# Optimization experiments

Measured on AMD Instinct MI355X. Metric: run time of the kernel, lower is better.

## Reference

```python
import jax, jax.numpy as jnp
import numpy as np
from jax import lax

W_SCALE = 0.1   # brevitas SignedBinaryWeightPerTensorConst default scaling_init
A_SCALE = 1.0   # SignedBinaryActPerTensorConst: min/max = -1/1 -> scale 1
BN_EPS = 1e-5


def _bin_w(w):
    # sign(w) * const scale, straight-through estimator (identity STE as in brevitas binary_sign_ste)
    q = jnp.where(w >= 0, W_SCALE, -W_SCALE).astype(w.dtype)
    return w + lax.stop_gradient(q - w)


def _bin_act(x):
    # QuantHardTanh with binary act quant: output is sign(x)*1, STE passes grad inside [-1,1]
    c = jnp.clip(x, -A_SCALE, A_SCALE)
    q = jnp.where(x >= 0, A_SCALE, -A_SCALE).astype(x.dtype)
    return c + lax.stop_gradient(q - c)


def _conv(x, w, b, stride=(1, 1), pad=((0, 0), (0, 0))):
    y = lax.conv_general_dilated(x, _bin_w(w), window_strides=stride, padding=pad,
                                 dimension_numbers=('NCHW', 'OIHW', 'NCHW'))
    return y + b[None, :, None, None]


def _bn(x, gamma, beta):
    # training-mode BatchNorm2d: batch statistics over (N, H, W)
    mu = jnp.mean(x, axis=(0, 2, 3), keepdims=True)
    var = jnp.var(x, axis=(0, 2, 3), keepdims=True)
    inv = lax.rsqrt(var + BN_EPS)
    return (x - mu) * inv * gamma[None, :, None, None] + beta[None, :, None, None]


def _pool2x1(x):
    # MaxPool2d((2,1)) with floor: drop trailing odd row
    N, C, H, W = x.shape
    h2 = H // 2
    return x[:, :, : 2 * h2].reshape(N, C, h2, 2, W).max(axis=3)


def setup_inputs() -> dict:
    key = jax.random.key(0)
    ks = jax.random.split(key, 10)
    nC = 128
    d = {
        'x':  jax.random.normal(ks[0], (64, 1, 16000, 1), jnp.float32),
        'w1': jax.random.normal(ks[1], (nC, 1, 84, 1), jnp.float32) * 0.05,
        'b1': jnp.zeros((nC,), jnp.float32),
        'g1': jnp.ones((nC,), jnp.float32), 'be1': jnp.zeros((nC,), jnp.float32),
        'w2': jax.random.normal(ks[2], (nC, nC, 4, 1), jnp.float32) * 0.05,
        'b2': jnp.zeros((nC,), jnp.float32),
        'g2': jnp.ones((nC,), jnp.float32), 'be2': jnp.zeros((nC,), jnp.float32),
        'w3': jax.random.normal(ks[3], (2 * nC, nC, 4, 1), jnp.float32) * 0.05,
        'b3': jnp.zeros((2 * nC,), jnp.float32),
        'g3': jnp.ones((2 * nC,), jnp.float32), 'be3': jnp.zeros((2 * nC,), jnp.float32),
        'w5': jax.random.normal(ks[4], (4 * nC, 2 * nC, 3, 1), jnp.float32) * 0.05,
        'b5': jnp.zeros((4 * nC,), jnp.float32),
        'g5': jnp.ones((4 * nC,), jnp.float32), 'be5': jnp.zeros((4 * nC,), jnp.float32),
        'wfc': jax.random.normal(ks[5], (35, 4 * nC * 249), jnp.float32) * 0.01,
    }
    return d


def reference(x, w1, b1, g1, be1, w2, b2, g2, be2, w3, b3, g3, be3,
              w5, b5, g5, be5, wfc):
    h = _conv(x, w1, b1, stride=(4, 1))                     # [B,128,3980,1]
    h = _pool2x1(_bin_act(_bn(h, g1, be1)))                 # [B,128,1990,1]
    h = _conv(h, w2, b2, pad=((2, 2), (0, 0)))              # [B,128,1991,1]
    h = _pool2x1(_bin_act(_bn(h, g2, be2)))                 # [B,128,995,1]
    h = _conv(h, w3, b3, pad=((1, 1), (0, 0)))              # [B,256,994,1]
    h = _pool2x1(_bin_act(_bn(h, g3, be3)))                 # [B,256,497,1]
    h = _conv(h, w5, b5, pad=((2, 2), (0, 0)))              # [B,512,499,1]
    h = _pool2x1(_bin_act(_bn(h, g5, be5)))                 # [B,512,249,1]
    h = h.reshape(h.shape[0], -1)                           # [B, 512*249]
    return h @ _bin_w(wfc).T                                # [B, 35]
```

## Files before the change

kernel.cpp:

```cpp
#include <hip/hip_runtime.h>
#include <stdint.h>


constexpr int Bn  = 64;
constexpr int H1  = 3980;
constexpr int J1  = 1990;
constexpr int H2o = 1991, J2 = 995;
constexpr int H3o = 994,  J3 = 497;
constexpr int H5o = 499,  J5 = 249;
constexpr int FCW = 249 * 8;

__global__ void binarize_all(const float* __restrict__ w2, const float* __restrict__ w3,
                             const float* __restrict__ w5, const float* __restrict__ w1,
                             uint64_t* __restrict__ wb2, uint64_t* __restrict__ wb3,
                             uint64_t* __restrict__ wb5, float* __restrict__ w1pk)
{
    int idx = blockIdx.x * 256 + threadIdx.x;
    if (idx < 1024) {
        int wdx = idx & 1, k = (idx >> 1) & 3, c = idx >> 3;
        uint64_t v = 0;
        for (int ci = 0; ci < 64; ++ci)
            if (w2[((size_t)c * 128 + (wdx * 64 + ci)) * 4 + k] >= 0.f) v |= 1ull << ci;
        wb2[idx] = v;
    } else if (idx < 3072) {
        int t = idx - 1024;
        int wdx = t & 1, k = (t >> 1) & 3, c = t >> 3;
        uint64_t v = 0;
        for (int ci = 0; ci < 64; ++ci)
            if (w3[((size_t)c * 128 + (wdx * 64 + ci)) * 4 + k] >= 0.f) v |= 1ull << ci;
        wb3[t] = v;
    } else if (idx < 9216) {
        int t = idx - 3072;
        int wdx = t & 3, k = (t >> 2) % 3, c = t / 12;
        uint64_t v = 0;
        for (int ci = 0; ci < 64; ++ci)
            if (w5[((size_t)c * 256 + (wdx * 64 + ci)) * 3 + k] >= 0.f) v |= 1ull << ci;
        wb5[t] = v;
    } else if (idx < 9216 + 10752) {
        int t  = idx - 9216;
        int G  = t / 672, r = t % 672;
        int kg = r >> 5;
        int e  = r & 31;
        int u  = e >> 2, jj = e & 3;
        w1pk[t] = (w1[(size_t)(G * 8 + u) * 84 + kg * 4 + jj] >= 0.f) ? 0.1f : -0.1f;
    }
}

__global__ __launch_bounds__(256) void binarize_fc(const float* __restrict__ wfc,
                                                   uint64_t* __restrict__ wbf)
{
    const int oc = blockIdx.x, wdx = blockIdx.y;
    const int wave = threadIdx.x >> 6, lane = threadIdx.x & 63;
    const int hh = wave * 64 + lane;
    const bool ok = hh < 249;
    const float* src = wfc + (size_t)oc * 127488 + (size_t)wdx * 64 * 249 + hh;
    uint64_t word = 0;
    #pragma unroll 8
    for (int c = 0; c < 64; ++c) {
        const float v = ok ? src[(size_t)c * 249] : -1.f;
        if (v >= 0.f) word |= 1ull << c;
    }
    if (ok) wbf[(size_t)oc * FCW + (size_t)hh * 8 + wdx] = word;
}

#define ROW_FMA(A, XV) \
    A[u] = fmaf(wv.x, XV.x, A[u]); A[u] = fmaf(wv.y, XV.y, A[u]); \
    A[u] = fmaf(wv.z, XV.z, A[u]); A[u] = fmaf(wv.w, XV.w, A[u]);
#define ROW_STAT(A, HOFF) { \
    const int h = h0 + (HOFF) + tid; \
    if (h < H1) { const float v = A[u] + bv; base[h] = v; \
                  s += (double)v; q += (double)v * v; } }

__global__ __launch_bounds__(256) void conv1_y1(
    const float* __restrict__ x, const float4* __restrict__ w1pk,
    const float* __restrict__ b1, float* __restrict__ y1,
    double2* __restrict__ part)
{
    __shared__ float4 xs4[2068];
    __shared__ float4 wl[336];
    __shared__ double2 statw[4][16];
    const int n   = blockIdx.y;
    const int bh  = blockIdx.x;
    const int h0  = bh << 11;
    const int z   = blockIdx.z;
    const int tid = threadIdx.x;
    const int wave = tid >> 6, lane = tid & 63;

    const float4* x4 = (const float4*)x + (size_t)n * 4000;
    for (int i = tid; i < 2068; i += 256) {
        const int gi = h0 + i;
        xs4[i] = (gi < 4000) ? x4[gi] : make_float4(0.f, 0.f, 0.f, 0.f);
    }
    const float4* wsrc = w1pk + (size_t)z * 336;
    for (int i = tid; i < 336; i += 256) wl[i] = wsrc[i];
    __syncthreads();

    for (int g = 0; g < 2; ++g) {
        float a0[8] = {0,0,0,0,0,0,0,0};
        float a1r[8] = {0,0,0,0,0,0,0,0};
        float a2[8] = {0,0,0,0,0,0,0,0};
        float a3[8] = {0,0,0,0,0,0,0,0};
        float a4[8] = {0,0,0,0,0,0,0,0};
        float a5[8] = {0,0,0,0,0,0,0,0};
        float a6[8] = {0,0,0,0,0,0,0,0};
        float a7[8] = {0,0,0,0,0,0,0,0};
        #pragma unroll 3
        for (int kg = 0; kg < 21; ++kg) {
            const float4 xv0 = xs4[tid + kg];
            const float4 xv1 = xs4[tid + 256 + kg];
            const float4 xv2 = xs4[tid + 512 + kg];
            const float4 xv3 = xs4[tid + 768 + kg];
            const float4 xv4 = xs4[tid + 1024 + kg];
            const float4 xv5 = xs4[tid + 1280 + kg];
            const float4 xv6 = xs4[tid + 1536 + kg];
            const float4 xv7 = xs4[tid + 1792 + kg];
            const float4* wk = &wl[(g * 21 + kg) * 8];
            #pragma unroll
            for (int u = 0; u < 8; ++u) {
                const float4 wv = wk[u];
                ROW_FMA(a0, xv0)
                ROW_FMA(a1r, xv1)
                ROW_FMA(a2, xv2)
                ROW_FMA(a3, xv3)
                ROW_FMA(a4, xv4)
                ROW_FMA(a5, xv5)
                ROW_FMA(a6, xv6)
                ROW_FMA(a7, xv7)
            }
        }
        #pragma unroll
        for (int u = 0; u < 8; ++u) {
            const int c = z * 16 + g * 8 + u;
            const float bv = b1[c];
            float* base = y1 + ((size_t)n * 128 + c) * H1;
            double s = 0.0, q = 0.0;
            ROW_STAT(a0, 0)
            ROW_STAT(a1r, 256)
            ROW_STAT(a2, 512)
            ROW_STAT(a3, 768)
            ROW_STAT(a4, 1024)
            ROW_STAT(a5, 1280)
            ROW_STAT(a6, 1536)
            ROW_STAT(a7, 1792)
            #pragma unroll
            for (int o = 32; o > 0; o >>= 1) {
                s += __shfl_xor(s, o, 64);
                q += __shfl_xor(q, o, 64);
            }
            if (lane == 0) statw[wave][g * 8 + u] = make_double2(s, q);
        }
    }
    __syncthreads();
    if (tid < 16) {
        const double2 p0 = statw[0][tid], p1v = statw[1][tid];
        const double2 p2 = statw[2][tid], p3  = statw[3][tid];
        part[((size_t)((n * 2 + bh) * 8 + z)) * 16 + tid] =
            make_double2(((p0.x + p1v.x) + p2.x) + p3.x,
                         ((p0.y + p1v.y) + p2.y) + p3.y);
    }
}

__global__ __launch_bounds__(128) void bn_reduce1(const double2* __restrict__ part,
                                                  float2* __restrict__ bnp)
{
    __shared__ double sS[128], sQ[128];
    const int c = blockIdx.x, t = threadIdx.x;
    const int z = c >> 4, cl = c & 15;
    const double2 p = part[((size_t)(t * 8 + z)) * 16 + cl];
    sS[t] = p.x; sQ[t] = p.y;
    __syncthreads();
    for (int o = 64; o > 0; o >>= 1) {
        if (t < o) { sS[t] += sS[t + o]; sQ[t] += sQ[t + o]; }
        __syncthreads();
    }
    if (t == 0) {
        const double N = (double)Bn * H1;
        const double mu  = sS[0] / N;
        const double var = sQ[0] / N - mu * mu;
        bnp[c] = make_float2((float)mu, (float)(1.0 / sqrt(var + 1e-5)));
    }
}

__global__ __launch_bounds__(256) void signpool1_y(
    const float* __restrict__ y1, const float2* __restrict__ bnp,
    const float* __restrict__ g1, const float* __restrict__ be1,
    uint64_t* __restrict__ a1)
{
    __shared__ float2 smi[128];
    __shared__ float  sg[128], sbe[128];
    const int n   = blockIdx.y;
    const int tid = threadIdx.x;
    if (tid < 128) { smi[tid] = bnp[tid]; sg[tid] = g1[tid]; sbe[tid] = be1[tid]; }
    __syncthreads();
    const int j2   = blockIdx.x * 128 + (tid & 127);
    const int half = tid >> 7;
    if (j2 >= 995) return;
    uint64_t wa = 0, wb = 0;
    for (int i = 0; i < 64; ++i) {
        const int c = half * 64 + i;
        const float4 v = *(const float4*)(y1 + ((size_t)n * 128 + c) * H1 + 4 * j2);
        const float2 mi = smi[c];
        const float gg = sg[c], bb = sbe[c];
        const float t0 = __fadd_rn(__fmul_rn(__fmul_rn(__fsub_rn(v.x, mi.x), mi.y), gg), bb);
        const float t1 = __fadd_rn(__fmul_rn(__fmul_rn(__fsub_rn(v.y, mi.x), mi.y), gg), bb);
        const float t2 = __fadd_rn(__fmul_rn(__fmul_rn(__fsub_rn(v.z, mi.x), mi.y), gg), bb);
        const float t3 = __fadd_rn(__fmul_rn(__fmul_rn(__fsub_rn(v.w, mi.x), mi.y), gg), bb);
        if ((t0 >= 0.f) || (t1 >= 0.f)) wa |= 1ull << i;
        if ((t2 >= 0.f) || (t3 >= 0.f)) wb |= 1ull << i;
    }
    uint64_t* dst = a1 + ((size_t)n * J1 + 2 * j2) * 2 + half;
    dst[0] = wa;
    dst[2] = wb;
}

template<int CINW, int KK, int PAD, int COUT>
__global__ __launch_bounds__(COUT) void bconv_stats(
    const uint64_t* __restrict__ ain, const uint64_t* __restrict__ wb,
    const int HIN, const int HOUT, int* __restrict__ part)
{
    __shared__ uint64_t rows[(64 + KK - 1) * CINW];
    const int n  = blockIdx.y;
    const int h0 = blockIdx.x << 6;
    const int c  = threadIdx.x;
    for (int i = c; i < (64 + KK - 1) * CINW; i += COUT) {
        int r = h0 - PAD + i / CINW;
        rows[i] = (r >= 0 && r < HIN) ? ain[((size_t)n * HIN + r) * CINW + (i % CINW)] : 0ull;
    }
    __syncthreads();
    uint64_t wreg[KK * CINW];
    #pragma unroll
    for (int i = 0; i < KK * CINW; ++i) wreg[i] = wb[(size_t)c * KK * CINW + i];
    int pcw[KK];
    #pragma unroll
    for (int k = 0; k < KK; ++k) {
        int pc = 0;
        #pragma unroll
        for (int wd = 0; wd < CINW; ++wd) pc += __popcll(wreg[k * CINW + wd]);
        pcw[k] = pc;
    }
    int sq = 0, sq2 = 0;
    const int hmax = min(64, HOUT - h0);
    for (int i = 0; i < hmax; ++i) {
        const int h = h0 + i;
        int X = 0;
        #pragma unroll
        for (int k = 0; k < KK; ++k)
            #pragma unroll
            for (int wd = 0; wd < CINW; ++wd)
                X += __popcll(rows[(i + k) * CINW + wd] ^ wreg[k * CINW + wd]);
        int q = 64 * CINW * KK - 2 * X;
        if (h < PAD || h > HIN + PAD - KK) {
            #pragma unroll
            for (int k = 0; k < KK; ++k)
                if (k < PAD - h || k >= HIN + PAD - h)
                    q -= 64 * CINW - 2 * pcw[k];
        }
        sq += q; sq2 += q * q;
    }
    const size_t blk = (size_t)n * gridDim.x + blockIdx.x;
    part[(blk * COUT + c) * 2 + 0] = sq;
    part[(blk * COUT + c) * 2 + 1] = sq2;
}

template<int CINW, int KK, int PAD, int COUT>
__global__ __launch_bounds__(COUT) void bconv_sign(
    const uint64_t* __restrict__ ain, const uint64_t* __restrict__ wb,
    const int HIN, const int HOUT, const int J,
    const float* __restrict__ bias, const float2* __restrict__ bnp,
    const float* __restrict__ g, const float* __restrict__ be,
    uint64_t* __restrict__ aout)
{
    constexpr int W = COUT / 64;
    __shared__ uint64_t rows[(64 + KK - 1) * CINW];
    const int n  = blockIdx.y;
    const int h0 = blockIdx.x << 6;
    const int c  = threadIdx.x;
    for (int i = c; i < (64 + KK - 1) * CINW; i += COUT) {
        int r = h0 - PAD + i / CINW;
        rows[i] = (r >= 0 && r < HIN) ? ain[((size_t)n * HIN + r) * CINW + (i % CINW)] : 0ull;
    }
    __syncthreads();
    uint64_t wreg[KK * CINW];
    #pragma unroll
    for (int i = 0; i < KK * CINW; ++i) wreg[i] = wb[(size_t)c * KK * CINW + i];
    int pcw[KK];
    #pragma unroll
    for (int k = 0; k < KK; ++k) {
        int pc = 0;
        #pragma unroll
        for (int wd = 0; wd < CINW; ++wd) pc += __popcll(wreg[k * CINW + wd]);
        pcw[k] = pc;
    }
    const float bb = bias[c], gg = g[c], bbe = be[c];
    const float2 mi = bnp[c];
    const int wv = c >> 6, lane = c & 63;
    uint64_t prev = 0;
    const int hmax = min(64, HOUT - h0);
    for (int i = 0; i < hmax; ++i) {
        const int h = h0 + i;
        int X = 0;
        #pragma unroll
        for (int k = 0; k < KK; ++k)
            #pragma unroll
            for (int wd = 0; wd < CINW; ++wd)
                X += __popcll(rows[(i + k) * CINW + wd] ^ wreg[k * CINW + wd]);
        int q = 64 * CINW * KK - 2 * X;
        if (h < PAD || h > HIN + PAD - KK) {
            #pragma unroll
            for (int k = 0; k < KK; ++k)
                if (k < PAD - h || k >= HIN + PAD - h)
                    q -= 64 * CINW - 2 * pcw[k];
        }
        const float y = __fadd_rn(__fmul_rn(0.1f, (float)q), bb);
        const float t = __fadd_rn(__fmul_rn(__fmul_rn(__fsub_rn(y, mi.x), mi.y), gg), bbe);
        const uint64_t word = __ballot(t >= 0.f);
        if (i & 1) {
            const int j = h >> 1;
            if (lane == 0 && j < J)
                aout[((size_t)n * J + j) * W + wv] = prev | word;
        } else {
            prev = word;
        }
    }
}

__global__ __launch_bounds__(256) void bn_reduce_q(
    const int* __restrict__ part, const int nblk, const int C,
    const double N, const float* __restrict__ bias, float2* __restrict__ bnp)
{
    __shared__ long long sS[256], sQ[256];
    const int c = blockIdx.x, t = threadIdx.x;
    long long Sq = 0, Sq2 = 0;
    for (int b = t; b < nblk; b += 256) {
        const int2 p = *(const int2*)(part + ((size_t)b * C + c) * 2);
        Sq += p.x; Sq2 += p.y;
    }
    sS[t] = Sq; sQ[t] = Sq2;
    __syncthreads();
    for (int o = 128; o > 0; o >>= 1) {
        if (t < o) { sS[t] += sS[t + o]; sQ[t] += sQ[t + o]; }
        __syncthreads();
    }
    if (t == 0) {
        const double bb = (double)bias[c];
        const double S  = 0.1 * (double)sS[0] + N * bb;
        const double SS = 0.01 * (double)sQ[0] + 0.2 * bb * (double)sS[0] + N * bb * bb;
        const double mu = S / N;
        const double var = SS / N - mu * mu;
        bnp[c] = make_float2((float)mu, (float)(1.0 / sqrt(var + 1e-5)));
    }
}

__global__ void fc_kernel(const uint64_t* __restrict__ a5, const uint64_t* __restrict__ wfcb,
                          float* __restrict__ out)
{
    const int n    = blockIdx.y;
    const int oc   = blockIdx.x * 4 + (threadIdx.x >> 6);
    const int lane = threadIdx.x & 63;
    if (oc >= 35) return;
    const uint64_t* arow = a5   + (size_t)n  * FCW;
    const uint64_t* wrow = wfcb + (size_t)oc * FCW;
    int X = 0;
    for (int i = lane; i < FCW; i += 64)
        X += __popcll(arow[i] ^ wrow[i]);
    for (int o = 32; o > 0; o >>= 1) X += __shfl_xor(X, o, 64);
    if (lane == 0) out[(size_t)n * 35 + oc] = 0.1f * (float)(127488 - 2 * X);
}

extern "C" void kernel_launch(void* const* d_in, const int* in_sizes, int n_in,
                              void* d_out, int out_size, void* d_ws, size_t ws_size,
                              hipStream_t stream)
{
    (void)in_sizes; (void)n_in; (void)out_size;
    const float* x   = (const float*)d_in[0];
    const float* w1  = (const float*)d_in[1];
    const float* b1  = (const float*)d_in[2];
    const float* g1  = (const float*)d_in[3];
    const float* be1 = (const float*)d_in[4];
    const float* w2  = (const float*)d_in[5];
    const float* b2  = (const float*)d_in[6];
    const float* g2  = (const float*)d_in[7];
    const float* be2 = (const float*)d_in[8];
    const float* w3  = (const float*)d_in[9];
    const float* b3  = (const float*)d_in[10];
    const float* g3  = (const float*)d_in[11];
    const float* be3 = (const float*)d_in[12];
    const float* w5  = (const float*)d_in[13];
    const float* b5  = (const float*)d_in[14];
    const float* g5  = (const float*)d_in[15];
    const float* be5 = (const float*)d_in[16];
    const float* wfc = (const float*)d_in[17];
    char* ws = (char*)d_ws;

    size_t cur = 0;
    auto take = [&](size_t bytes) {
        size_t r = cur;
        cur = (cur + bytes + 255) & ~(size_t)255;
        return r;
    };
    const size_t off_y1 = take(130416640);
    float*    y1  = (float*)(ws + off_y1);
    int*      pq  = (int*)(ws + off_y1 + 35651584);
    uint64_t* a1  = (uint64_t*)(ws + take(2037760));
    uint64_t* a2  = (uint64_t*)(ws + take(1018880));
    uint64_t* a3  = (uint64_t*)(ws + take(1017856));
    uint64_t* a5  = (uint64_t*)(ws + take(1019904));
    uint64_t* wb2 = (uint64_t*)(ws + take(8192));
    uint64_t* wb3 = (uint64_t*)(ws + take(16384));
    uint64_t* wb5 = (uint64_t*)(ws + take(49152));
    uint64_t* wbf = (uint64_t*)(ws + take(557760));
    float*    w1pk = (float*)(ws + take(43008));
    double2*  p1  = (double2*)(ws + take(262144));
    float2*   bnp1 = (float2*)(ws + take(1024));
    float2*   bnp2 = (float2*)(ws + take(1024));
    float2*   bnp3 = (float2*)(ws + take(2048));
    float2*   bnp5 = (float2*)(ws + take(4096));
    if (cur > ws_size) return;

    hipLaunchKernelGGL(binarize_all, dim3(78), dim3(256), 0, stream,
                       w2, w3, w5, w1, wb2, wb3, wb5, w1pk);
    hipLaunchKernelGGL(binarize_fc, dim3(35, 8), dim3(256), 0, stream, wfc, wbf);
    hipLaunchKernelGGL(conv1_y1, dim3(2, 64, 8), dim3(256), 0, stream,
                       x, (const float4*)w1pk, b1, y1, p1);
    hipLaunchKernelGGL(bn_reduce1, dim3(128), dim3(128), 0, stream, p1, bnp1);
    hipLaunchKernelGGL(signpool1_y, dim3(8, 64), dim3(256), 0, stream,
                       y1, bnp1, g1, be1, a1);
    hipLaunchKernelGGL((bconv_stats<2, 4, 2, 128>), dim3(32, 64), dim3(128), 0, stream,
                       a1, wb2, J1, H2o, pq);
    hipLaunchKernelGGL(bn_reduce_q, dim3(128), dim3(256), 0, stream,
                       pq, 2048, 128, (double)Bn * H2o, b2, bnp2);
    hipLaunchKernelGGL((bconv_sign<2, 4, 2, 128>), dim3(32, 64), dim3(128), 0, stream,
                       a1, wb2, J1, H2o, J2, b2, bnp2, g2, be2, a2);
    hipLaunchKernelGGL((bconv_stats<2, 4, 1, 256>), dim3(16, 64), dim3(256), 0, stream,
                       a2, wb3, J2, H3o, pq);
    hipLaunchKernelGGL(bn_reduce_q, dim3(256), dim3(256), 0, stream,
                       pq, 1024, 256, (double)Bn * H3o, b3, bnp3);
    hipLaunchKernelGGL((bconv_sign<2, 4, 1, 256>), dim3(16, 64), dim3(256), 0, stream,
                       a2, wb3, J2, H3o, J3, b3, bnp3, g3, be3, a3);
    hipLaunchKernelGGL((bconv_stats<4, 3, 2, 512>), dim3(8, 64), dim3(512), 0, stream,
                       a3, wb5, J3, H5o, pq);
    hipLaunchKernelGGL(bn_reduce_q, dim3(512), dim3(256), 0, stream,
                       pq, 512, 512, (double)Bn * H5o, b5, bnp5);
    hipLaunchKernelGGL((bconv_sign<4, 3, 2, 512>), dim3(8, 64), dim3(512), 0, stream,
                       a3, wb5, J3, H5o, J5, b5, bnp5, g5, be5, a5);
    hipLaunchKernelGGL(fc_kernel, dim3(9, 64), dim3(256), 0, stream,
                       a5, wbf, (float*)d_out);
}
```

Measured before the change: 327.9 us.

## Replace BN reduce kernels with sharded atomics and merge weight prep kernels

The stats kernels now atomically accumulate integer sum and sum-of-squares into 16 sharded 64-bit counters, replacing per-block partial writes. The sign kernels read the shards directly and compute mean and inverse std inline, so the three separate bn_reduce_q launches are removed. The two weight binarization kernels are merged into one prep kernel that also zeroes the accumulators. This cuts four kernel launches and a partial-sum round trip, at the cost of atomic contention and redundant per-block stat recomputation.

```diff
diff --git a/kernel.cpp b/kernel.cpp
--- a/kernel.cpp
+++ b/kernel.cpp
@@ -9,58 +9,68 @@
 constexpr int H3o = 994,  J3 = 497;
 constexpr int H5o = 499,  J5 = 249;
 constexpr int FCW = 249 * 8;
-
-__global__ void binarize_all(const float* __restrict__ w2, const float* __restrict__ w3,
-                             const float* __restrict__ w5, const float* __restrict__ w1,
-                             uint64_t* __restrict__ wb2, uint64_t* __restrict__ wb3,
-                             uint64_t* __restrict__ wb5, float* __restrict__ w1pk)
-{
-    int idx = blockIdx.x * 256 + threadIdx.x;
-    if (idx < 1024) {
-        int wdx = idx & 1, k = (idx >> 1) & 3, c = idx >> 3;
-        uint64_t v = 0;
-        for (int ci = 0; ci < 64; ++ci)
-            if (w2[((size_t)c * 128 + (wdx * 64 + ci)) * 4 + k] >= 0.f) v |= 1ull << ci;
-        wb2[idx] = v;
-    } else if (idx < 3072) {
-        int t = idx - 1024;
-        int wdx = t & 1, k = (t >> 1) & 3, c = t >> 3;
-        uint64_t v = 0;
-        for (int ci = 0; ci < 64; ++ci)
-            if (w3[((size_t)c * 128 + (wdx * 64 + ci)) * 4 + k] >= 0.f) v |= 1ull << ci;
-        wb3[t] = v;
-    } else if (idx < 9216) {
-        int t = idx - 3072;
-        int wdx = t & 3, k = (t >> 2) % 3, c = t / 12;
-        uint64_t v = 0;
-        for (int ci = 0; ci < 64; ++ci)
-            if (w5[((size_t)c * 256 + (wdx * 64 + ci)) * 3 + k] >= 0.f) v |= 1ull << ci;
-        wb5[t] = v;
-    } else if (idx < 9216 + 10752) {
-        int t  = idx - 9216;
-        int G  = t / 672, r = t % 672;
-        int kg = r >> 5;
-        int e  = r & 31;
-        int u  = e >> 2, jj = e & 3;
-        w1pk[t] = (w1[(size_t)(G * 8 + u) * 84 + kg * 4 + jj] >= 0.f) ? 0.1f : -0.1f;
-    }
-}
-
-__global__ __launch_bounds__(256) void binarize_fc(const float* __restrict__ wfc,
-                                                   uint64_t* __restrict__ wbf)
-{
-    const int oc = blockIdx.x, wdx = blockIdx.y;
-    const int wave = threadIdx.x >> 6, lane = threadIdx.x & 63;
-    const int hh = wave * 64 + lane;
-    const bool ok = hh < 249;
-    const float* src = wfc + (size_t)oc * 127488 + (size_t)wdx * 64 * 249 + hh;
-    uint64_t word = 0;
-    #pragma unroll 8
-    for (int c = 0; c < 64; ++c) {
-        const float v = ok ? src[(size_t)c * 249] : -1.f;
-        if (v >= 0.f) word |= 1ull << c;
-    }
-    if (ok) wbf[(size_t)oc * FCW + (size_t)hh * 8 + wdx] = word;
+constexpr int NSH = 16;
+constexpr int QS2 = 0;
+constexpr int QS3 = 4096;
+constexpr int QS5 = 12288;
+constexpr int QS_TOTAL = 28672;
+
+__global__ __launch_bounds__(256) void prep_all(
+    const float* __restrict__ w2, const float* __restrict__ w3,
+    const float* __restrict__ w5, const float* __restrict__ wfc,
+    const float* __restrict__ w1,
+    uint64_t* __restrict__ wb2, uint64_t* __restrict__ wb3,
+    uint64_t* __restrict__ wb5, uint64_t* __restrict__ wbf,
+    float* __restrict__ w1pk, unsigned long long* __restrict__ qs)
+{
+    const int bx  = blockIdx.x;
+    const int idx = bx * 256 + threadIdx.x;
+    if (idx < QS_TOTAL) qs[idx] = 0ull;
+
+    if (bx < 78) {
+        if (idx < 1024) {
+            int wdx = idx & 1, k = (idx >> 1) & 3, c = idx >> 3;
+            uint64_t v = 0;
+            for (int ci = 0; ci < 64; ++ci)
+                if (w2[((size_t)c * 128 + (wdx * 64 + ci)) * 4 + k] >= 0.f) v |= 1ull << ci;
+            wb2[idx] = v;
+        } else if (idx < 3072) {
+            int t = idx - 1024;
+            int wdx = t & 1, k = (t >> 1) & 3, c = t >> 3;
+            uint64_t v = 0;
+            for (int ci = 0; ci < 64; ++ci)
+                if (w3[((size_t)c * 128 + (wdx * 64 + ci)) * 4 + k] >= 0.f) v |= 1ull << ci;
+            wb3[t] = v;
+        } else if (idx < 9216) {
+            int t = idx - 3072;
+            int wdx = t & 3, k = (t >> 2) % 3, c = t / 12;
+            uint64_t v = 0;
+            for (int ci = 0; ci < 64; ++ci)
+                if (w5[((size_t)c * 256 + (wdx * 64 + ci)) * 3 + k] >= 0.f) v |= 1ull << ci;
+            wb5[t] = v;
+        } else if (idx < 9216 + 10752) {
+            int t  = idx - 9216;
+            int G  = t / 672, r = t % 672;
+            int kg = r >> 5;
+            int e  = r & 31;
+            int u  = e >> 2, jj = e & 3;
+            w1pk[t] = (w1[(size_t)(G * 8 + u) * 84 + kg * 4 + jj] >= 0.f) ? 0.1f : -0.1f;
+        }
+    } else {
+        const int t = bx - 78;
+        const int oc = t >> 3, wdx = t & 7;
+        const int wave = threadIdx.x >> 6, lane = threadIdx.x & 63;
+        const int hh = wave * 64 + lane;
+        const bool ok = hh < 249;
+        const float* src = wfc + (size_t)oc * 127488 + (size_t)wdx * 64 * 249 + hh;
+        uint64_t word = 0;
+        #pragma unroll 8
+        for (int c = 0; c < 64; ++c) {
+            const float v = ok ? src[(size_t)c * 249] : -1.f;
+            if (v >= 0.f) word |= 1ull << c;
+        }
+        if (ok) wbf[(size_t)oc * FCW + (size_t)hh * 8 + wdx] = word;
+    }
 }
 
 #define ROW_FMA(A, XV) \
@@ -216,7 +226,7 @@
 template<int CINW, int KK, int PAD, int COUT>
 __global__ __launch_bounds__(COUT) void bconv_stats(
     const uint64_t* __restrict__ ain, const uint64_t* __restrict__ wb,
-    const int HIN, const int HOUT, int* __restrict__ part)
+    const int HIN, const int HOUT, unsigned long long* __restrict__ qs)
 {
     __shared__ uint64_t rows[(64 + KK - 1) * CINW];
     const int n  = blockIdx.y;
@@ -257,16 +267,16 @@
         }
         sq += q; sq2 += q * q;
     }
-    const size_t blk = (size_t)n * gridDim.x + blockIdx.x;
-    part[(blk * COUT + c) * 2 + 0] = sq;
-    part[(blk * COUT + c) * 2 + 1] = sq2;
+    const int sh = (blockIdx.x + blockIdx.y) & (NSH - 1);
+    atomicAdd(&qs[((size_t)sh * COUT + c) * 2 + 0], (unsigned long long)(long long)sq);
+    atomicAdd(&qs[((size_t)sh * COUT + c) * 2 + 1], (unsigned long long)(long long)sq2);
 }
 
 template<int CINW, int KK, int PAD, int COUT>
 __global__ __launch_bounds__(COUT) void bconv_sign(
     const uint64_t* __restrict__ ain, const uint64_t* __restrict__ wb,
-    const int HIN, const int HOUT, const int J,
-    const float* __restrict__ bias, const float2* __restrict__ bnp,
+    const int HIN, const int HOUT, const int J, const double N,
+    const float* __restrict__ bias, const unsigned long long* __restrict__ qs,
     const float* __restrict__ g, const float* __restrict__ be,
     uint64_t* __restrict__ aout)
 {
@@ -279,6 +289,18 @@
         int r = h0 - PAD + i / CINW;
         rows[i] = (r >= 0 && r < HIN) ? ain[((size_t)n * HIN + r) * CINW + (i % CINW)] : 0ull;
     }
+    long long Sq = 0, Sq2 = 0;
+    #pragma unroll
+    for (int s = 0; s < NSH; ++s) {
+        Sq  += (long long)qs[((size_t)s * COUT + c) * 2 + 0];
+        Sq2 += (long long)qs[((size_t)s * COUT + c) * 2 + 1];
+    }
+    const double bb_d = (double)bias[c];
+    const double S  = 0.1 * (double)Sq + N * bb_d;
+    const double SS = 0.01 * (double)Sq2 + 0.2 * bb_d * (double)Sq + N * bb_d * bb_d;
+    const double mu = S / N;
+    const double var = SS / N - mu * mu;
+    const float2 mi = make_float2((float)mu, (float)(1.0 / sqrt(var + 1e-5)));
     __syncthreads();
     uint64_t wreg[KK * CINW];
     #pragma unroll
@@ -292,7 +314,6 @@
         pcw[k] = pc;
     }
     const float bb = bias[c], gg = g[c], bbe = be[c];
-    const float2 mi = bnp[c];
     const int wv = c >> 6, lane = c & 63;
     uint64_t prev = 0;
     const int hmax = min(64, HOUT - h0);
@@ -321,33 +342,6 @@
         } else {
             prev = word;
         }
-    }
-}
-
-__global__ __launch_bounds__(256) void bn_reduce_q(
-    const int* __restrict__ part, const int nblk, const int C,
-    const double N, const float* __restrict__ bias, float2* __restrict__ bnp)
-{
-    __shared__ long long sS[256], sQ[256];
-    const int c = blockIdx.x, t = threadIdx.x;
-    long long Sq = 0, Sq2 = 0;
-    for (int b = t; b < nblk; b += 256) {
-        const int2 p = *(const int2*)(part + ((size_t)b * C + c) * 2);
-        Sq += p.x; Sq2 += p.y;
-    }
-    sS[t] = Sq; sQ[t] = Sq2;
-    __syncthreads();
-    for (int o = 128; o > 0; o >>= 1) {
-        if (t < o) { sS[t] += sS[t + o]; sQ[t] += sQ[t + o]; }
-        __syncthreads();
-    }
-    if (t == 0) {
-        const double bb = (double)bias[c];
-        const double S  = 0.1 * (double)sS[0] + N * bb;
-        const double SS = 0.01 * (double)sQ[0] + 0.2 * bb * (double)sS[0] + N * bb * bb;
-        const double mu = S / N;
-        const double var = SS / N - mu * mu;
-        bnp[c] = make_float2((float)mu, (float)(1.0 / sqrt(var + 1e-5)));
     }
 }
 
@@ -400,7 +394,6 @@
     };
     const size_t off_y1 = take(130416640);
     float*    y1  = (float*)(ws + off_y1);
-    int*      pq  = (int*)(ws + off_y1 + 35651584);
     uint64_t* a1  = (uint64_t*)(ws + take(2037760));
     uint64_t* a2  = (uint64_t*)(ws + take(1018880));
     uint64_t* a3  = (uint64_t*)(ws + take(1017856));
@@ -411,38 +404,29 @@
     uint64_t* wbf = (uint64_t*)(ws + take(557760));
     float*    w1pk = (float*)(ws + take(43008));
     double2*  p1  = (double2*)(ws + take(262144));
+    unsigned long long* qs = (unsigned long long*)(ws + take(QS_TOTAL * 8));
     float2*   bnp1 = (float2*)(ws + take(1024));
-    float2*   bnp2 = (float2*)(ws + take(1024));
-    float2*   bnp3 = (float2*)(ws + take(2048));
-    float2*   bnp5 = (float2*)(ws + take(4096));
     if (cur > ws_size) return;
 
-    hipLaunchKernelGGL(binarize_all, dim3(78), dim3(256), 0, stream,
-                       w2, w3, w5, w1, wb2, wb3, wb5, w1pk);
-    hipLaunchKernelGGL(binarize_fc, dim3(35, 8), dim3(256), 0, stream, wfc, wbf);
+    hipLaunchKernelGGL(prep_all, dim3(358), dim3(256), 0, stream,
+                       w2, w3, w5, wfc, w1, wb2, wb3, wb5, wbf, w1pk, qs);
     hipLaunchKernelGGL(conv1_y1, dim3(2, 64, 8), dim3(256), 0, stream,
                        x, (const float4*)w1pk, b1, y1, p1);
     hipLaunchKernelGGL(bn_reduce1, dim3(128), dim3(128), 0, stream, p1, bnp1);
     hipLaunchKernelGGL(signpool1_y, dim3(8, 64), dim3(256), 0, stream,
                        y1, bnp1, g1, be1, a1);
     hipLaunchKernelGGL((bconv_stats<2, 4, 2, 128>), dim3(32, 64), dim3(128), 0, stream,
-                       a1, wb2, J1, H2o, pq);
-    hipLaunchKernelGGL(bn_reduce_q, dim3(128), dim3(256), 0, stream,
-                       pq, 2048, 128, (double)Bn * H2o, b2, bnp2);
+                       a1, wb2, J1, H2o, qs + QS2);
     hipLaunchKernelGGL((bconv_sign<2, 4, 2, 128>), dim3(32, 64), dim3(128), 0, stream,
-                       a1, wb2, J1, H2o, J2, b2, bnp2, g2, be2, a2);
+                       a1, wb2, J1, H2o, J2, (double)Bn * H2o, b2, qs + QS2, g2, be2, a2);
     hipLaunchKernelGGL((bconv_stats<2, 4, 1, 256>), dim3(16, 64), dim3(256), 0, stream,
-                       a2, wb3, J2, H3o, pq);
-    hipLaunchKernelGGL(bn_reduce_q, dim3(256), dim3(256), 0, stream,
-                       pq, 1024, 256, (double)Bn * H3o, b3, bnp3);
+                       a2, wb3, J2, H3o, qs + QS3);
     hipLaunchKernelGGL((bconv_sign<2, 4, 1, 256>), dim3(16, 64), dim3(256), 0, stream,
-                       a2, wb3, J2, H3o, J3, b3, bnp3, g3, be3, a3);
+                       a2, wb3, J2, H3o, J3, (double)Bn * H3o, b3, qs + QS3, g3, be3, a3);
     hipLaunchKernelGGL((bconv_stats<4, 3, 2, 512>), dim3(8, 64), dim3(512), 0, stream,
-                       a3, wb5, J3, H5o, pq);
-    hipLaunchKernelGGL(bn_reduce_q, dim3(512), dim3(256), 0, stream,
-                       pq, 512, 512, (double)Bn * H5o, b5, bnp5);
+                       a3, wb5, J3, H5o, qs + QS5);
     hipLaunchKernelGGL((bconv_sign<4, 3, 2, 512>), dim3(8, 64), dim3(512), 0, stream,
-                       a3, wb5, J3, H5o, J5, b5, bnp5, g5, be5, a5);
+                       a3, wb5, J3, H5o, J5, (double)Bn * H5o, b5, qs + QS5, g5, be5, a5);
     hipLaunchKernelGGL(fc_kernel, dim3(9, 64), dim3(256), 0, stream,
                        a5, wbf, (float*)d_out);
 }
```

New measurement: 310.9 us. -5.2%, faster.
